# Optimization experiments

Hardware: AMD Instinct MI355X
Metric: run time of the kernel (lower is better)

Reference implementation:

```python
import jax, jax.numpy as jnp
import numpy as np

B, S, D = 2, 2048, 2048
H, G = 32, 8            # n_head, n_kv_groups
DH = D // H             # 64
HG = H // G             # heads per group = 4


def setup_inputs() -> dict:
    key = jax.random.key(0)
    ks = jax.random.split(key, 7)
    kv_dim = G * DH
    return {
        "q": jax.random.normal(ks[0], (B, S, D), jnp.float32),
        "k": jax.random.normal(ks[1], (B, S, D), jnp.float32),
        "v": jax.random.normal(ks[2], (B, S, D), jnp.float32),
        "mask": jnp.tril(jnp.ones((S, S), jnp.bool_)),  # causal
        "w_q": jax.random.normal(ks[3], (D, D), jnp.float32) * 0.02,
        "w_k": jax.random.normal(ks[4], (kv_dim, D), jnp.float32) * 0.02,
        "w_v": jax.random.normal(ks[5], (kv_dim, D), jnp.float32) * 0.02,
        "w_out": jax.random.normal(ks[6], (D, D), jnp.float32) * 0.02,
    }


def reference(q, k, v, mask, w_q, w_k, w_v, w_out):
    scale = 1.0 / np.sqrt(DH).astype(np.float32)
    # projections (F.linear: x @ W.T)
    qp = (q @ w_q.T).reshape(B, S, G, HG, DH)   # [b s g h d]
    kp = (k @ w_k.T).reshape(B, S, G, DH)       # [b t g d]
    vp = (v @ w_v.T).reshape(B, S, G, DH)
    # grouped attention scores [b g h s t]
    scores = jnp.einsum('bsghd,btgd->bghst', qp, kp) * scale
    scores = jnp.where(mask[None, None, None], scores, jnp.float32(-jnp.inf))
    attn = jax.nn.softmax(scores, axis=-1)
    out = jnp.einsum('bghst,btgd->bsghd', attn, vp).reshape(B, S, D)
    return out @ w_out.T
```

## Files before the change

### kernel.cpp

```cpp
#include <hip/hip_runtime.h>
#include <hip/hip_bf16.h>
#include <stdint.h>

#define B_SZ 2
#define S_LEN 2048
#define D_MODEL 2048
#define NH 32
#define NG 8
#define HGRP 4
#define DHEAD 64
#define KV_DIM 512
#define M_TOK 4096
#define KVB 64
#define QBLK 256
#define N_ITEMS2 768

typedef __attribute__((ext_vector_type(8))) short bf16x8;
typedef __attribute__((ext_vector_type(4))) float f32x4;
typedef __attribute__((ext_vector_type(16))) float f32x16;

__device__ inline unsigned short f2bf(float x) {
    uint32_t u = __builtin_bit_cast(uint32_t, x);
    uint32_t r = (u + 0x7fffu + ((u >> 16) & 1u)) >> 16;
    return (unsigned short)r;
}

__device__ inline uint32_t cvtpk(float lo, float hi) {
    uint32_t r;
    asm("v_cvt_pk_bf16_f32 %0, %1, %2" : "=v"(r) : "v"(lo), "v"(hi));
    return r;
}

__device__ inline void plswap(uint32_t& a, uint32_t& b) {
    asm volatile("v_permlane32_swap_b32 %0, %1" : "+v"(a), "+v"(b));
}

__device__ inline float bf2f(unsigned short u) {
    uint32_t x = ((uint32_t)u) << 16;
    return __builtin_bit_cast(float, x);
}

__device__ inline void async_copy16(const void* g, void* l) {
    __builtin_amdgcn_global_load_lds(
        (const __attribute__((address_space(1))) void*)g,
        (__attribute__((address_space(3))) void*)l,
        16, 0, 0);
}

__device__ inline void gbar() {
    asm volatile("" ::: "memory");
    __builtin_amdgcn_s_barrier();
    asm volatile("" ::: "memory");
}
__device__ inline void lgkm0() {
    asm volatile("s_waitcnt lgkmcnt(0)" ::: "memory");
    __builtin_amdgcn_sched_barrier(0);
}

__global__ __launch_bounds__(256) void cvt_all(const float* __restrict__ q,
                                               const float* __restrict__ k,
                                               const float* __restrict__ v,
                                               const float* __restrict__ wq,
                                               const float* __restrict__ wk,
                                               const float* __restrict__ wv,
                                               const float* __restrict__ wo,
                                               unsigned short* __restrict__ qb,
                                               unsigned short* __restrict__ kb,
                                               unsigned short* __restrict__ vb,
                                               unsigned short* __restrict__ wqb,
                                               unsigned short* __restrict__ wkvb,
                                               unsigned short* __restrict__ wob,
                                               unsigned int* __restrict__ cnt) {
    const int i = blockIdx.x * 256 + threadIdx.x;
    if (i == 0) *cnt = 0u;
    const float* src; unsigned short* dst; int j;
    if (i < 1048576)      { src = q;  dst = qb;  j = i; }
    else if (i < 2097152) { src = k;  dst = kb;  j = i - 1048576; }
    else if (i < 3145728) { src = v;  dst = vb;  j = i - 2097152; }
    else if (i < 3670016) { src = wq; dst = wqb; j = i - 3145728; }
    else if (i < 3801088) { src = wk; dst = wkvb; j = i - 3670016; }
    else if (i < 3932160) { src = wv; dst = wkvb + (size_t)KV_DIM * D_MODEL; j = i - 3801088; }
    else                  { src = wo; dst = wob; j = i - 3932160; }
    const float4* p = reinterpret_cast<const float4*>(src) + (size_t)j * 2;
    float4 a = p[0], b = p[1];
    union { unsigned short u[8]; uint4 v4; } r;
    r.u[0] = f2bf(a.x); r.u[1] = f2bf(a.y); r.u[2] = f2bf(a.z); r.u[3] = f2bf(a.w);
    r.u[4] = f2bf(b.x); r.u[5] = f2bf(b.y); r.u[6] = f2bf(b.z); r.u[7] = f2bf(b.w);
    reinterpret_cast<uint4*>(dst)[j] = r.v4;
}

#define SCALE_Q 0.1803368867f
#define GK 2048

__global__ __launch_bounds__(512, 2) void gemm8p(const unsigned short* __restrict__ Aq,
                                                 const unsigned short* __restrict__ Ak,
                                                 const unsigned short* __restrict__ Av,
                                                 const unsigned short* __restrict__ Bq,
                                                 const unsigned short* __restrict__ Bkv,
                                                 unsigned short* __restrict__ out_q,
                                                 unsigned short* __restrict__ out_k,
                                                 unsigned short* __restrict__ out_v) {
    __shared__ __align__(16) char lds[131072];

    const int tid = threadIdx.x;
    const int lane = tid & 63;
    const int w = tid >> 6;
    const int wm = w >> 2, wn = w & 3;
    const int l15 = lane & 15, l4 = lane >> 4;

    int bid = blockIdx.x;
    bid = (bid & 7) * 24 + (bid >> 3);
    const int mb = bid & 15, nb = bid >> 4;
    const int m0 = mb * 256;

    const unsigned short* Ap;
    const unsigned short* Bp;
    int mode = 0, n0q = 0;
    if (nb < 8) {
        Ap = Aq; Bp = Bq + (size_t)(nb * 256) * GK; mode = 0; n0q = nb * 256;
    } else if (nb < 10) {
        Ap = Ak; Bp = Bkv + (size_t)((nb - 8) * 256) * GK; mode = 1; n0q = (nb - 8) * 256;
    } else {
        Ap = Av; Bp = Bkv + (size_t)((nb - 10) * 256 + 512) * GK; mode = 2; n0q = (nb - 10) * 256;
    }

    const int srow = tid >> 3;
    const int gcol = (((tid & 7) * 16) ^ ((srow & 7) << 4)) >> 1;
    char* const myl = lds + tid * 16;

    auto stageA = [&](int tile, int half) {
        char* dst = myl + (tile & 1) * 32768 + half * 16384;
        const unsigned short* src = Ap + (size_t)(m0 + half * 128 + srow) * GK + tile * 64 + gcol;
        async_copy16(src, dst);
        async_copy16(src + (size_t)64 * GK, dst + 8192);
    };
    auto stageB = [&](int tile, int half) {
        char* dst = myl + 65536 + (tile & 1) * 32768 + half * 16384;
        const unsigned short* src = Bp + (size_t)(half * 128 + srow) * GK + tile * 64 + gcol;
        async_copy16(src, dst);
        async_copy16(src + (size_t)64 * GK, dst + 8192);
    };

    bf16x8 af[4][2], bf[4][2];
    auto loadA = [&](int buf, int mhalf) {
        const char* base = lds + buf * 32768;
#pragma unroll
        for (int mi = 0; mi < 4; ++mi) {
            const int r = wm * 128 + mhalf * 64 + mi * 16 + l15;
#pragma unroll
            for (int ks = 0; ks < 2; ++ks)
                af[mi][ks] = *reinterpret_cast<const bf16x8*>(
                    base + r * 128 + ((ks * 64 + l4 * 16) ^ ((r & 7) << 4)));
        }
    };
    auto loadB = [&](int buf, int nhalf) {
        const char* base = lds + 65536 + buf * 32768;
#pragma unroll
        for (int ni2 = 0; ni2 < 2; ++ni2) {
            const int ni = nhalf * 2 + ni2;
            const int r = wn * 64 + ni * 16 + l15;
#pragma unroll
            for (int ks = 0; ks < 2; ++ks)
                bf[ni][ks] = *reinterpret_cast<const bf16x8*>(
                    base + r * 128 + ((ks * 64 + l4 * 16) ^ ((r & 7) << 4)));
        }
    };

    f32x4 acc[8][4] = {};
    auto mfma16 = [&](int mq, int nq) {
        __builtin_amdgcn_s_setprio(1);
#pragma unroll
        for (int mi = 0; mi < 4; ++mi)
#pragma unroll
            for (int ni2 = 0; ni2 < 2; ++ni2)
#pragma unroll
                for (int ks = 0; ks < 2; ++ks)
                    acc[mq * 4 + mi][nq * 2 + ni2] = __builtin_amdgcn_mfma_f32_16x16x32_bf16(
                        af[mi][ks], bf[nq * 2 + ni2][ks], acc[mq * 4 + mi][nq * 2 + ni2], 0, 0, 0);
        __builtin_amdgcn_s_setprio(0);
    };

    stageA(0, 0); stageA(0, 1); stageB(0, 0); stageB(0, 1); stageB(1, 0); stageB(1, 1);
    asm volatile("s_waitcnt vmcnt(4)" ::: "memory");
    gbar();

    for (int i = 0; i < 16; ++i) {
        const int u = 2 * i;
        const bool nl = (i < 15);
        loadA(0, 0); loadB(0, 0); stageA(u + 1, 0);
        gbar(); lgkm0(); mfma16(0, 0); gbar();
        loadB(0, 1); stageA(u + 1, 1);
        gbar(); lgkm0(); mfma16(0, 1); gbar();
        loadA(0, 1); if (nl) stageB(u + 2, 0);
        gbar(); lgkm0(); mfma16(1, 0); gbar();
        if (nl) stageB(u + 2, 1);
        gbar(); mfma16(1, 1);
        if (nl) asm volatile("s_waitcnt vmcnt(4)" ::: "memory");
        else    asm volatile("s_waitcnt vmcnt(0)" ::: "memory");
        gbar();
        loadA(1, 0); loadB(1, 0); if (nl) stageA(u + 2, 0);
        gbar(); lgkm0(); mfma16(0, 0); gbar();
        loadB(1, 1); if (nl) stageA(u + 2, 1);
        gbar(); lgkm0(); mfma16(0, 1); gbar();
        loadA(1, 1); if (nl) stageB(u + 3, 0);
        gbar(); lgkm0(); mfma16(1, 0); gbar();
        if (nl) stageB(u + 3, 1);
        gbar(); mfma16(1, 1);
        if (nl) asm volatile("s_waitcnt vmcnt(4)" ::: "memory");
        gbar();
    }

    if (mode == 0) {
#pragma unroll
        for (int mi = 0; mi < 8; ++mi) {
            const int row = m0 + wm * 128 + mi * 16 + l4 * 4;
#pragma unroll
            for (int ni = 0; ni < 4; ++ni) {
                const int col = n0q + wn * 64 + ni * 16 + l15;
#pragma unroll
                for (int r = 0; r < 4; ++r)
                    out_q[(size_t)(row + r) * D_MODEL + col] = f2bf(acc[mi][ni][r] * SCALE_Q);
            }
        }
    } else if (mode == 1) {
#pragma unroll
        for (int mi = 0; mi < 8; ++mi) {
            const int row = m0 + wm * 128 + mi * 16 + l4 * 4;
#pragma unroll
            for (int ni = 0; ni < 4; ++ni) {
                const int col = n0q + wn * 64 + ni * 16 + l15;
#pragma unroll
                for (int r = 0; r < 4; ++r)
                    out_k[(size_t)(row + r) * KV_DIM + col] = f2bf(acc[mi][ni][r]);
            }
        }
    } else {
        const int bb = m0 >> 11;
#pragma unroll
        for (int mi = 0; mi < 8; ++mi) {
            const int tok = (m0 & 2047) + wm * 128 + mi * 16 + l4 * 4;
#pragma unroll
            for (int ni = 0; ni < 4; ++ni) {
                const int c = n0q + wn * 64 + ni * 16 + l15;
                const int g = c >> 6, dh = c & 63;
                uint2 pk;
                pk.x = cvtpk(acc[mi][ni][0], acc[mi][ni][1]);
                pk.y = cvtpk(acc[mi][ni][2], acc[mi][ni][3]);
                *reinterpret_cast<uint2*>(out_v + (size_t)((bb * NG + g) * DHEAD + dh) * S_LEN + tok) = pk;
            }
        }
    }
}

__global__ __launch_bounds__(512, 1) void gemm8o(const unsigned short* __restrict__ A,
                                                 const unsigned short* __restrict__ B,
                                                 float* __restrict__ C) {
    __shared__ __align__(16) char lds[98304];

    const int tid = threadIdx.x;
    const int lane = tid & 63;
    const int w = tid >> 6;
    const int wm = w >> 1, wn = w & 1;
    const int l15 = lane & 15, l4 = lane >> 4;

    int bid = blockIdx.x;
    bid = (bid & 7) * 32 + (bid >> 3);
    const int mb = bid & 15, nb = bid >> 4;
    const int m0 = mb * 256, n0 = nb * 128;
    const unsigned short* Bp = B + (size_t)n0 * GK;

    const int srow = tid >> 3;
    const int gcol = (((tid & 7) * 16) ^ ((srow & 7) << 4)) >> 1;

    auto stageA = [&](int tile, int half) {
        char* dst = lds + (tile & 1) * 32768 + half * 16384 + tid * 16;
        const unsigned short* src = A + (size_t)(m0 + half * 128 + srow) * GK + tile * 64 + gcol;
        async_copy16(src, dst);
        async_copy16(src + (size_t)64 * GK, dst + 8192);
    };
    auto stageB = [&](int tile, int half) {
        char* dst = lds + 65536 + (tile & 1) * 16384 + half * 8192 + tid * 16;
        const unsigned short* src = Bp + (size_t)(half * 64 + srow) * GK + tile * 64 + gcol;
        async_copy16(src, dst);
    };

    bf16x8 af[2][2], bf[4][2];
    auto loadA2 = [&](int buf, int mhalf) {
        const char* base = lds + buf * 32768;
#pragma unroll
        for (int mi = 0; mi < 2; ++mi) {
            const int r = wm * 64 + mhalf * 32 + mi * 16 + l15;
#pragma unroll
            for (int ks = 0; ks < 2; ++ks)
                af[mi][ks] = *reinterpret_cast<const bf16x8*>(
                    base + r * 128 + ((ks * 64 + l4 * 16) ^ ((r & 7) << 4)));
        }
    };
    auto loadB2 = [&](int buf, int nhalf) {
        const char* base = lds + 65536 + buf * 16384;
#pragma unroll
        for (int ni2 = 0; ni2 < 2; ++ni2) {
            const int ni = nhalf * 2 + ni2;
            const int r = wn * 64 + ni * 16 + l15;
#pragma unroll
            for (int ks = 0; ks < 2; ++ks)
                bf[ni][ks] = *reinterpret_cast<const bf16x8*>(
                    base + r * 128 + ((ks * 64 + l4 * 16) ^ ((r & 7) << 4)));
        }
    };

    f32x4 acc[4][4] = {};
    auto mfma8 = [&](int mq, int nq) {
        __builtin_amdgcn_s_setprio(1);
#pragma unroll
        for (int mi = 0; mi < 2; ++mi)
#pragma unroll
            for (int ni2 = 0; ni2 < 2; ++ni2)
#pragma unroll
                for (int ks = 0; ks < 2; ++ks)
                    acc[mq * 2 + mi][nq * 2 + ni2] = __builtin_amdgcn_mfma_f32_16x16x32_bf16(
                        af[mi][ks], bf[nq * 2 + ni2][ks], acc[mq * 2 + mi][nq * 2 + ni2], 0, 0, 0);
        __builtin_amdgcn_s_setprio(0);
    };

    stageA(0, 0); stageA(0, 1); stageB(0, 0); stageB(0, 1); stageB(1, 0); stageB(1, 1);
    asm volatile("s_waitcnt vmcnt(2)" ::: "memory");
    gbar();

    for (int i = 0; i < 16; ++i) {
        const int u = 2 * i;
        const bool nl = (i < 15);
        loadA2(0, 0); loadB2(0, 0); stageA(u + 1, 0);
        gbar(); lgkm0(); mfma8(0, 0); gbar();
        loadB2(0, 1); stageA(u + 1, 1);
        gbar(); lgkm0(); mfma8(0, 1); gbar();
        loadA2(0, 1); if (nl) stageB(u + 2, 0);
        gbar(); lgkm0(); mfma8(1, 0); gbar();
        if (nl) stageB(u + 2, 1);
        gbar(); mfma8(1, 1);
        if (nl) asm volatile("s_waitcnt vmcnt(2)" ::: "memory");
        else    asm volatile("s_waitcnt vmcnt(0)" ::: "memory");
        gbar();
        loadA2(1, 0); loadB2(1, 0); if (nl) stageA(u + 2, 0);
        gbar(); lgkm0(); mfma8(0, 0); gbar();
        loadB2(1, 1); if (nl) stageA(u + 2, 1);
        gbar(); lgkm0(); mfma8(0, 1); gbar();
        loadA2(1, 1); if (nl) stageB(u + 3, 0);
        gbar(); lgkm0(); mfma8(1, 0); gbar();
        if (nl) stageB(u + 3, 1);
        gbar(); mfma8(1, 1);
        if (nl) asm volatile("s_waitcnt vmcnt(2)" ::: "memory");
        gbar();
    }

#pragma unroll
    for (int mi = 0; mi < 4; ++mi) {
        const int row = m0 + wm * 64 + mi * 16 + l4 * 4;
#pragma unroll
        for (int ni = 0; ni < 4; ++ni) {
            const int col = n0 + wn * 64 + ni * 16 + l15;
#pragma unroll
            for (int r = 0; r < 4; ++r)
                C[(size_t)(row + r) * D_MODEL + col] = acc[mi][ni][r];
        }
    }
}

__constant__ unsigned char cls2_qi[12]   = {7,7,3,6,6,5,5,2,4,4,1,0};
__constant__ unsigned char cls2_half[12] = {0,1,0,0,1,0,1,0,0,1,0,0};

__global__ __launch_bounds__(512, 4) void attn3_kernel(const unsigned short* __restrict__ qp,
                                                       const unsigned short* __restrict__ kp,
                                                       const unsigned short* __restrict__ vpT,
                                                       unsigned short* __restrict__ attn_out,
                                                       unsigned int* __restrict__ counter,
                                                       unsigned short* __restrict__ partO,
                                                       float* __restrict__ ml) {
    __shared__ __align__(16) unsigned short Ks[2][KVB * 64];
    __shared__ __align__(16) unsigned short Vs[2][KVB * 64];
    __shared__ int s_item;

    const int tid = threadIdx.x;
    const int lane = tid & 63;
    const int w = tid >> 6;
    const int l31 = lane & 31, hi = lane >> 5;
    const int sr = tid >> 3, sc = tid & 7;
    const int sgcol = (((sc * 16) ^ ((sr & 7) << 4)) >> 1);
    char* const kdst0 = (char*)Ks[0] + tid * 16;
    char* const kdst1 = (char*)Ks[1] + tid * 16;
    char* const vdst0 = (char*)Vs[0] + tid * 16;
    char* const vdst1 = (char*)Vs[1] + tid * 16;

    for (;;) {
        if (tid == 0) s_item = (int)atomicAdd(counter, 1u);
        __syncthreads();
        const int item = s_item;
        if (item >= N_ITEMS2) break;
        const int slot = item >> 6;
        const int bh = item & 63;
        const int qi = cls2_qi[slot];
        const int half = cls2_half[slot];
        const bool split = qi >= 4;
        const int b = bh >> 5, head = bh & 31, g = head >> 2;
        const int s0 = qi * QBLK;
        const int m = s0 + w * 32 + l31;
        const int mmaxw = s0 + w * 32 + 31;

        int j0, j1;
        if (split) { j0 = half * 2 * (qi + 1); j1 = j0 + 2 * (qi + 1); }
        else       { j0 = 0;                   j1 = 4 * (qi + 1); }

        bf16x8 qf[4];
        {
            const unsigned short* qrow = qp + (size_t)(b * S_LEN + m) * D_MODEL + head * DHEAD + hi * 8;
#pragma unroll
            for (int k = 0; k < 4; ++k)
                qf[k] = *reinterpret_cast<const bf16x8*>(qrow + k * 16);
        }

        const unsigned short* kbase = kp + (size_t)(b * S_LEN + sr) * KV_DIM + g * DHEAD + sgcol;
        const unsigned short* vbase = vpT + (size_t)((b * NG + g) * DHEAD + sr) * S_LEN + sgcol;

        float mrun = -1e30f, lrun = 0.f;
        f32x16 o0 = {}, o1 = {};

        async_copy16(kbase + (size_t)j0 * KVB * KV_DIM, kdst0);
        async_copy16(vbase + j0 * KVB, vdst0);
        asm volatile("s_waitcnt vmcnt(0)" ::: "memory");
        gbar();

        for (int j = j0; j < j1; ++j) {
            const int cur = (j - j0) & 1;
            const int t0 = j * KVB;
            if (j + 1 < j1) {
                async_copy16(kbase + (size_t)(j + 1) * KVB * KV_DIM, cur ? kdst0 : kdst1);
                async_copy16(vbase + (j + 1) * KVB, cur ? vdst0 : vdst1);
            }

            const bool tt0 = (t0 <= mmaxw);
            const bool tt1 = (t0 + 32 <= mmaxw);
            if (tt0) {
                const char* Kb = (const char*)Ks[cur];
                const char* Vb = (const char*)Vs[cur];
                const int rswz0 = (l31 & 7) << 4;

                f32x16 s0v = {}, s1v = {};
#pragma unroll
                for (int k = 0; k < 4; ++k) {
                    const int coff = k * 32 + hi * 16;
                    const bf16x8 kf0 = *reinterpret_cast<const bf16x8*>(
                        Kb + l31 * 128 + (coff ^ rswz0));
                    s0v = __builtin_amdgcn_mfma_f32_32x32x16_bf16(kf0, qf[k], s0v, 0, 0, 0);
                    if (tt1) {
                        const bf16x8 kf1 = *reinterpret_cast<const bf16x8*>(
                            Kb + (32 + l31) * 128 + (coff ^ rswz0));
                        s1v = __builtin_amdgcn_mfma_f32_32x32x16_bf16(kf1, qf[k], s1v, 0, 0, 0);
                    }
                }

                const bool msk = (t0 + KVB - 1) > (s0 + w * 32);
                float rmax = -1e30f;
                if (msk) {
#pragma unroll
                    for (int r = 0; r < 16; ++r) {
                        const int tloc = (r & 3) + 8 * (r >> 2) + 4 * hi;
                        float v = s0v[r];
                        if (t0 + tloc > m) v = -1e30f;
                        s0v[r] = v;
                        rmax = fmaxf(rmax, v);
                    }
                    if (tt1) {
#pragma unroll
                        for (int r = 0; r < 16; ++r) {
                            const int tloc = 32 + (r & 3) + 8 * (r >> 2) + 4 * hi;
                            float v = s1v[r];
                            if (t0 + tloc > m) v = -1e30f;
                            s1v[r] = v;
                            rmax = fmaxf(rmax, v);
                        }
                    }
                } else {
#pragma unroll
                    for (int r = 0; r < 16; ++r)
                        rmax = fmaxf(rmax, s0v[r]);
                    if (tt1) {
#pragma unroll
                        for (int r = 0; r < 16; ++r)
                            rmax = fmaxf(rmax, s1v[r]);
                    }
                }
                rmax = fmaxf(rmax, __shfl_xor(rmax, 32, 64));
                if (!__all(rmax <= mrun + 8.0f)) {
                    const float mnew = fmaxf(mrun, rmax);
                    const float corr = __builtin_amdgcn_exp2f(mrun - mnew);
                    lrun *= corr;
#pragma unroll
                    for (int r = 0; r < 16; ++r) { o0[r] *= corr; o1[r] *= corr; }
                    mrun = mnew;
                }
                float rs = 0.f;
#pragma unroll
                for (int r = 0; r < 16; ++r) {
                    const float p = __builtin_amdgcn_exp2f(s0v[r] - mrun);
                    s0v[r] = p;
                    rs += p;
                }
                if (tt1) {
#pragma unroll
                    for (int r = 0; r < 16; ++r) {
                        const float p = __builtin_amdgcn_exp2f(s1v[r] - mrun);
                        s1v[r] = p;
                        rs += p;
                    }
                }
                rs += __shfl_xor(rs, 32, 64);
                lrun += rs;

#pragma unroll
                for (int c = 0; c < 4; ++c) {
                    if (c >= 2 && !tt1) break;
                    const f32x16& sv = (c >> 1) ? s1v : s0v;
                    const int h8 = (c & 1) * 8;
                    uint32_t a0 = cvtpk(sv[h8 + 0], sv[h8 + 1]);
                    uint32_t a1 = cvtpk(sv[h8 + 2], sv[h8 + 3]);
                    uint32_t b0 = cvtpk(sv[h8 + 4], sv[h8 + 5]);
                    uint32_t b1 = cvtpk(sv[h8 + 6], sv[h8 + 7]);
                    plswap(a0, b0); plswap(a1, b1);
                    union { uint32_t w4[4]; bf16x8 v; } pf;
                    pf.w4[0] = a0; pf.w4[1] = a1; pf.w4[2] = b0; pf.w4[3] = b1;
                    const int coff = c * 32 + hi * 16;
                    const bf16x8 vf0 = *reinterpret_cast<const bf16x8*>(
                        Vb + l31 * 128 + (coff ^ rswz0));
                    o0 = __builtin_amdgcn_mfma_f32_32x32x16_bf16(vf0, pf.v, o0, 0, 0, 0);
                    const bf16x8 vf1 = *reinterpret_cast<const bf16x8*>(
                        Vb + (32 + l31) * 128 + (coff ^ rswz0));
                    o1 = __builtin_amdgcn_mfma_f32_32x32x16_bf16(vf1, pf.v, o1, 0, 0, 0);
                }
            }
            asm volatile("s_waitcnt vmcnt(0)" ::: "memory");
            gbar();
        }

        if (split) {
            const int pb = ((bh << 2) + (qi - 4)) * 2 + half;
            const int mrow = w * 32 + l31;
            if (hi == 0) {
                ml[pb * 512 + mrow] = mrun;
                ml[pb * 512 + 256 + mrow] = lrun;
            }
            unsigned short* dst = partO + (size_t)pb * 16384 + mrow * 64 + hi * 4;
#pragma unroll
            for (int qd = 0; qd < 4; ++qd) {
                uint2 pk0, pk1;
                pk0.x = cvtpk(o0[4 * qd + 0], o0[4 * qd + 1]);
                pk0.y = cvtpk(o0[4 * qd + 2], o0[4 * qd + 3]);
                pk1.x = cvtpk(o1[4 * qd + 0], o1[4 * qd + 1]);
                pk1.y = cvtpk(o1[4 * qd + 2], o1[4 * qd + 3]);
                *reinterpret_cast<uint2*>(dst + 8 * qd) = pk0;
                *reinterpret_cast<uint2*>(dst + 32 + 8 * qd) = pk1;
            }
        } else {
            const float inv = 1.0f / lrun;
            unsigned short* dst = attn_out + (size_t)(b * S_LEN + m) * D_MODEL + head * DHEAD + hi * 4;
#pragma unroll
            for (int qd = 0; qd < 4; ++qd) {
                uint2 pk0, pk1;
                pk0.x = cvtpk(o0[4 * qd + 0] * inv, o0[4 * qd + 1] * inv);
                pk0.y = cvtpk(o0[4 * qd + 2] * inv, o0[4 * qd + 3] * inv);
                pk1.x = cvtpk(o1[4 * qd + 0] * inv, o1[4 * qd + 1] * inv);
                pk1.y = cvtpk(o1[4 * qd + 2] * inv, o1[4 * qd + 3] * inv);
                *reinterpret_cast<uint2*>(dst + 8 * qd) = pk0;
                *reinterpret_cast<uint2*>(dst + 32 + 8 * qd) = pk1;
            }
        }
    }
}

__global__ __launch_bounds__(512) void merge2_kernel(const unsigned short* __restrict__ partO,
                                                     const float* __restrict__ ml,
                                                     unsigned short* __restrict__ attn_out) {
    const int blk = blockIdx.x;
    const int bh = blk >> 2;
    const int qi = (blk & 3) + 4;
    const int b = bh >> 5, head = bh & 31;
    const int s0 = qi * QBLK;
    const int tid = threadIdx.x;
    const int row = tid >> 1, dh0 = (tid & 1) * 32;
    const int pb0 = blk * 2, pb1 = pb0 + 1;

    const float m0 = ml[pb0 * 512 + row], l0 = ml[pb0 * 512 + 256 + row];
    const float m1 = ml[pb1 * 512 + row], l1 = ml[pb1 * 512 + 256 + row];
    const float M = fmaxf(m0, m1);
    float w0 = __builtin_amdgcn_exp2f(m0 - M);
    float w1 = __builtin_amdgcn_exp2f(m1 - M);
    const float inv = 1.0f / (l0 * w0 + l1 * w1);
    w0 *= inv; w1 *= inv;

    const uint4* p0 = reinterpret_cast<const uint4*>(partO + (size_t)pb0 * 16384 + row * 64 + dh0);
    const uint4* p1 = reinterpret_cast<const uint4*>(partO + (size_t)pb1 * 16384 + row * 64 + dh0);
    unsigned short* dst = attn_out + (size_t)(b * S_LEN + s0 + row) * D_MODEL + head * DHEAD + dh0;
#pragma unroll
    for (int c = 0; c < 4; ++c) {
        union { unsigned short u[8]; uint4 v; } ua, ub, uo;
        ua.v = p0[c]; ub.v = p1[c];
#pragma unroll
        for (int e = 0; e < 8; e += 2) {
            float x0 = bf2f(ua.u[e]) * w0 + bf2f(ub.u[e]) * w1;
            float x1 = bf2f(ua.u[e + 1]) * w0 + bf2f(ub.u[e + 1]) * w1;
            reinterpret_cast<uint32_t*>(uo.u)[e >> 1] = cvtpk(x0, x1);
        }
        reinterpret_cast<uint4*>(dst)[c] = uo.v;
    }
}

extern "C" void kernel_launch(void* const* d_in, const int* in_sizes, int n_in,
                              void* d_out, int out_size, void* d_ws, size_t ws_size,
                              hipStream_t stream) {
    const float* q     = (const float*)d_in[0];
    const float* k     = (const float*)d_in[1];
    const float* v     = (const float*)d_in[2];
    const float* w_q   = (const float*)d_in[4];
    const float* w_k   = (const float*)d_in[5];
    const float* w_v   = (const float*)d_in[6];
    const float* w_out = (const float*)d_in[7];

    char* ws = (char*)d_ws;
    size_t off = 0;
    auto alloc = [&](size_t n) { char* p = ws + off; off += (n + 255) & ~(size_t)255; return p; };
    unsigned short* qb   = (unsigned short*)alloc((size_t)M_TOK * D_MODEL * 2);
    unsigned short* kb   = (unsigned short*)alloc((size_t)M_TOK * D_MODEL * 2);
    unsigned short* vb   = (unsigned short*)alloc((size_t)M_TOK * D_MODEL * 2);
    unsigned short* wqb  = (unsigned short*)alloc((size_t)D_MODEL * D_MODEL * 2);
    unsigned short* wkvb = (unsigned short*)alloc((size_t)2 * KV_DIM * D_MODEL * 2);
    unsigned short* wob  = (unsigned short*)alloc((size_t)D_MODEL * D_MODEL * 2);
    unsigned short* qpb  = (unsigned short*)alloc((size_t)M_TOK * D_MODEL * 2);
    unsigned short* kpb  = (unsigned short*)alloc((size_t)M_TOK * KV_DIM * 2);
    unsigned short* vtb  = (unsigned short*)alloc((size_t)M_TOK * KV_DIM * 2);
    unsigned short* aob  = (unsigned short*)alloc((size_t)M_TOK * D_MODEL * 2);
    float*          mlb  = (float*)alloc((size_t)512 * 512 * 4);
    unsigned int*   cnt  = (unsigned int*)alloc(256);

    cvt_all<<<dim3(17408), dim3(256), 0, stream>>>(q, k, v, w_q, w_k, w_v, w_out,
                                                   qb, kb, vb, wqb, wkvb, wob, cnt);

    gemm8p<<<dim3(192), dim3(512), 0, stream>>>(qb, kb, vb, wqb, wkvb, qpb, kpb, vtb);

    attn3_kernel<<<dim3(768), dim3(512), 0, stream>>>(qpb, kpb, vtb, aob, cnt, qb, mlb);
    merge2_kernel<<<dim3(256), dim3(512), 0, stream>>>(qb, mlb, aob);

    gemm8o<<<dim3(256), dim3(512), 0, stream>>>(aob, wob, (float*)d_out);
}
```

Baseline: 189.3 us.

## Split causal attention into finer equal-size KV chunks with multi-part merge

Replaces the two-way split of the longest query blocks with a schedule of 1280 work items. Each item covers at most about 8 KV tiles, and every query block from index 2 upward is split into 2 to 4 partial results. A new merge kernel combines up to 4 partials using their running max and sum. The aim is to balance load across workgroups and shrink the tail, at the cost of more partial-output traffic and merge work. It also restructures the row max and sum reductions as trees, and reuses the kb/qb workspace buffers for the partials and the max/sum values.

```diff
diff --git a/kernel.cpp b/kernel.cpp
--- a/kernel.cpp
+++ b/kernel.cpp
@@ -13,7 +13,7 @@
 #define M_TOK 4096
 #define KVB 64
 #define QBLK 256
-#define N_ITEMS2 768
+#define N_ITEMS 1280
 
 typedef __attribute__((ext_vector_type(8))) short bf16x8;
 typedef __attribute__((ext_vector_type(4))) float f32x4;
@@ -55,6 +55,22 @@
 __device__ inline void lgkm0() {
     asm volatile("s_waitcnt lgkmcnt(0)" ::: "memory");
     __builtin_amdgcn_sched_barrier(0);
+}
+
+__device__ inline float vmax16(const f32x16& v) {
+    float a0 = fmaxf(v[0], v[1]), a1 = fmaxf(v[2], v[3]);
+    float a2 = fmaxf(v[4], v[5]), a3 = fmaxf(v[6], v[7]);
+    float a4 = fmaxf(v[8], v[9]), a5 = fmaxf(v[10], v[11]);
+    float a6 = fmaxf(v[12], v[13]), a7 = fmaxf(v[14], v[15]);
+    float b0 = fmaxf(a0, a1), b1 = fmaxf(a2, a3);
+    float b2 = fmaxf(a4, a5), b3 = fmaxf(a6, a7);
+    return fmaxf(fmaxf(b0, b1), fmaxf(b2, b3));
+}
+__device__ inline float vsum16(const f32x16& v) {
+    float a0 = v[0] + v[1], a1 = v[2] + v[3], a2 = v[4] + v[5], a3 = v[6] + v[7];
+    float a4 = v[8] + v[9], a5 = v[10] + v[11], a6 = v[12] + v[13], a7 = v[14] + v[15];
+    float b0 = a0 + a1, b1 = a2 + a3, b2 = a4 + a5, b3 = a6 + a7;
+    return (b0 + b1) + (b2 + b3);
 }
 
 __global__ __launch_bounds__(256) void cvt_all(const float* __restrict__ q,
@@ -366,10 +382,14 @@
     }
 }
 
-__constant__ unsigned char cls2_qi[12]   = {7,7,3,6,6,5,5,2,4,4,1,0};
-__constant__ unsigned char cls2_half[12] = {0,1,0,0,1,0,1,0,0,1,0,0};
-
-__global__ __launch_bounds__(512, 4) void attn3_kernel(const unsigned short* __restrict__ qp,
+__constant__ unsigned char sl_qi[20] = {7,7,7,7, 5,5,5, 3,3, 1, 6,6,6,6, 4,4,4, 2,2, 0};
+__constant__ unsigned char sl_j0[20] = {0,8,16,24, 0,8,16, 0,8, 0, 0,7,14,21, 0,7,14, 0,6, 0};
+__constant__ unsigned char sl_j1[20] = {8,16,24,32, 8,16,24, 8,16, 8, 7,14,21,28, 7,14,20, 6,12, 4};
+__constant__ unsigned char sl_pt[20] = {0,1,2,3, 0,1,2, 0,1, 0, 0,1,2,3, 0,1,2, 0,1, 0};
+__constant__ unsigned char pb_base[6] = {16,14,11,8,4,0};
+__constant__ unsigned char np_tab[6]  = {2,2,3,3,4,4};
+
+__global__ __launch_bounds__(512, 4) void attn7_kernel(const unsigned short* __restrict__ qp,
                                                        const unsigned short* __restrict__ kp,
                                                        const unsigned short* __restrict__ vpT,
                                                        unsigned short* __restrict__ attn_out,
@@ -395,20 +415,19 @@
         if (tid == 0) s_item = (int)atomicAdd(counter, 1u);
         __syncthreads();
         const int item = s_item;
-        if (item >= N_ITEMS2) break;
-        const int slot = item >> 6;
+        if (item >= N_ITEMS) break;
+        const int slot = item / 64;
         const int bh = item & 63;
-        const int qi = cls2_qi[slot];
-        const int half = cls2_half[slot];
-        const bool split = qi >= 4;
+        const int qi = sl_qi[slot];
+        const int j0 = sl_j0[slot];
+        const int j1 = sl_j1[slot];
+        const int part = sl_pt[slot];
+        const bool merged = (qi >= 2);
         const int b = bh >> 5, head = bh & 31, g = head >> 2;
         const int s0 = qi * QBLK;
         const int m = s0 + w * 32 + l31;
-        const int mmaxw = s0 + w * 32 + 31;
-
-        int j0, j1;
-        if (split) { j0 = half * 2 * (qi + 1); j1 = j0 + 2 * (qi + 1); }
-        else       { j0 = 0;                   j1 = 4 * (qi + 1); }
+        const int mmin = s0 + w * 32;
+        const int mmaxw = mmin + 31;
 
         bf16x8 qf[4];
         {
@@ -458,37 +477,23 @@
                     }
                 }
 
-                const bool msk = (t0 + KVB - 1) > (s0 + w * 32);
-                float rmax = -1e30f;
+                const bool msk = (t0 + KVB - 1) > mmin;
                 if (msk) {
 #pragma unroll
                     for (int r = 0; r < 16; ++r) {
                         const int tloc = (r & 3) + 8 * (r >> 2) + 4 * hi;
-                        float v = s0v[r];
-                        if (t0 + tloc > m) v = -1e30f;
-                        s0v[r] = v;
-                        rmax = fmaxf(rmax, v);
+                        if (t0 + tloc > m) s0v[r] = -1e30f;
                     }
                     if (tt1) {
 #pragma unroll
                         for (int r = 0; r < 16; ++r) {
                             const int tloc = 32 + (r & 3) + 8 * (r >> 2) + 4 * hi;
-                            float v = s1v[r];
-                            if (t0 + tloc > m) v = -1e30f;
-                            s1v[r] = v;
-                            rmax = fmaxf(rmax, v);
+                            if (t0 + tloc > m) s1v[r] = -1e30f;
                         }
                     }
-                } else {
-#pragma unroll
-                    for (int r = 0; r < 16; ++r)
-                        rmax = fmaxf(rmax, s0v[r]);
-                    if (tt1) {
-#pragma unroll
-                        for (int r = 0; r < 16; ++r)
-                            rmax = fmaxf(rmax, s1v[r]);
-                    }
                 }
+                float rmax = vmax16(s0v);
+                if (tt1) rmax = fmaxf(rmax, vmax16(s1v));
                 rmax = fmaxf(rmax, __shfl_xor(rmax, 32, 64));
                 if (!__all(rmax <= mrun + 8.0f)) {
                     const float mnew = fmaxf(mrun, rmax);
@@ -498,21 +503,16 @@
                     for (int r = 0; r < 16; ++r) { o0[r] *= corr; o1[r] *= corr; }
                     mrun = mnew;
                 }
-                float rs = 0.f;
-#pragma unroll
-                for (int r = 0; r < 16; ++r) {
-                    const float p = __builtin_amdgcn_exp2f(s0v[r] - mrun);
-                    s0v[r] = p;
-                    rs += p;
+#pragma unroll
+                for (int r = 0; r < 16; ++r)
+                    s0v[r] = __builtin_amdgcn_exp2f(s0v[r] - mrun);
+                if (tt1) {
+#pragma unroll
+                    for (int r = 0; r < 16; ++r)
+                        s1v[r] = __builtin_amdgcn_exp2f(s1v[r] - mrun);
                 }
-                if (tt1) {
-#pragma unroll
-                    for (int r = 0; r < 16; ++r) {
-                        const float p = __builtin_amdgcn_exp2f(s1v[r] - mrun);
-                        s1v[r] = p;
-                        rs += p;
-                    }
-                }
+                float rs = vsum16(s0v);
+                if (tt1) rs += vsum16(s1v);
                 rs += __shfl_xor(rs, 32, 64);
                 lrun += rs;
 
@@ -541,8 +541,8 @@
             gbar();
         }
 
-        if (split) {
-            const int pb = ((bh << 2) + (qi - 4)) * 2 + half;
+        if (merged) {
+            const int pb = bh * 18 + pb_base[qi - 2] + part;
             const int mrow = w * 32 + l31;
             if (hi == 0) {
                 ml[pb * 512 + mrow] = mrun;
@@ -576,39 +576,56 @@
     }
 }
 
-__global__ __launch_bounds__(512) void merge2_kernel(const unsigned short* __restrict__ partO,
+__global__ __launch_bounds__(512) void merge5_kernel(const unsigned short* __restrict__ partO,
                                                      const float* __restrict__ ml,
                                                      unsigned short* __restrict__ attn_out) {
     const int blk = blockIdx.x;
-    const int bh = blk >> 2;
-    const int qi = (blk & 3) + 4;
+    const int bh = blk / 6;
+    const int qi = 2 + (blk - bh * 6);
+    const int np = np_tab[qi - 2];
+    const int pb = bh * 18 + pb_base[qi - 2];
     const int b = bh >> 5, head = bh & 31;
     const int s0 = qi * QBLK;
     const int tid = threadIdx.x;
     const int row = tid >> 1, dh0 = (tid & 1) * 32;
-    const int pb0 = blk * 2, pb1 = pb0 + 1;
-
-    const float m0 = ml[pb0 * 512 + row], l0 = ml[pb0 * 512 + 256 + row];
-    const float m1 = ml[pb1 * 512 + row], l1 = ml[pb1 * 512 + 256 + row];
-    const float M = fmaxf(m0, m1);
-    float w0 = __builtin_amdgcn_exp2f(m0 - M);
-    float w1 = __builtin_amdgcn_exp2f(m1 - M);
-    const float inv = 1.0f / (l0 * w0 + l1 * w1);
-    w0 *= inv; w1 *= inv;
-
-    const uint4* p0 = reinterpret_cast<const uint4*>(partO + (size_t)pb0 * 16384 + row * 64 + dh0);
-    const uint4* p1 = reinterpret_cast<const uint4*>(partO + (size_t)pb1 * 16384 + row * 64 + dh0);
+
+    float mv[4], lv[4];
+#pragma unroll
+    for (int i = 0; i < 4; ++i) {
+        if (i < np) { mv[i] = ml[(pb + i) * 512 + row]; lv[i] = ml[(pb + i) * 512 + 256 + row]; }
+        else        { mv[i] = -1e30f; lv[i] = 0.f; }
+    }
+    const float M = fmaxf(fmaxf(mv[0], mv[1]), fmaxf(mv[2], mv[3]));
+    float wgt[4];
+    float denom = 0.f;
+#pragma unroll
+    for (int i = 0; i < 4; ++i) {
+        wgt[i] = (i < np) ? __builtin_amdgcn_exp2f(mv[i] - M) : 0.f;
+        denom += lv[i] * wgt[i];
+    }
+    const float inv = 1.0f / denom;
+#pragma unroll
+    for (int i = 0; i < 4; ++i) wgt[i] *= inv;
+
     unsigned short* dst = attn_out + (size_t)(b * S_LEN + s0 + row) * D_MODEL + head * DHEAD + dh0;
 #pragma unroll
     for (int c = 0; c < 4; ++c) {
-        union { unsigned short u[8]; uint4 v; } ua, ub, uo;
-        ua.v = p0[c]; ub.v = p1[c];
-#pragma unroll
-        for (int e = 0; e < 8; e += 2) {
-            float x0 = bf2f(ua.u[e]) * w0 + bf2f(ub.u[e]) * w1;
-            float x1 = bf2f(ua.u[e + 1]) * w0 + bf2f(ub.u[e + 1]) * w1;
-            reinterpret_cast<uint32_t*>(uo.u)[e >> 1] = cvtpk(x0, x1);
-        }
+        float x[8] = {};
+#pragma unroll
+        for (int i = 0; i < 4; ++i) {
+            if (i < np) {
+                union { unsigned short u[8]; uint4 v; } ua;
+                ua.v = reinterpret_cast<const uint4*>(
+                    partO + (size_t)(pb + i) * 16384 + row * 64 + dh0)[c];
+#pragma unroll
+                for (int e = 0; e < 8; ++e)
+                    x[e] += bf2f(ua.u[e]) * wgt[i];
+            }
+        }
+        union { unsigned short u[8]; uint4 v; } uo;
+#pragma unroll
+        for (int e = 0; e < 8; e += 2)
+            reinterpret_cast<uint32_t*>(uo.u)[e >> 1] = cvtpk(x[e], x[e + 1]);
         reinterpret_cast<uint4*>(dst)[c] = uo.v;
     }
 }
@@ -637,7 +654,6 @@
     unsigned short* kpb  = (unsigned short*)alloc((size_t)M_TOK * KV_DIM * 2);
     unsigned short* vtb  = (unsigned short*)alloc((size_t)M_TOK * KV_DIM * 2);
     unsigned short* aob  = (unsigned short*)alloc((size_t)M_TOK * D_MODEL * 2);
-    float*          mlb  = (float*)alloc((size_t)512 * 512 * 4);
     unsigned int*   cnt  = (unsigned int*)alloc(256);
 
     cvt_all<<<dim3(17408), dim3(256), 0, stream>>>(q, k, v, w_q, w_k, w_v, w_out,
@@ -645,8 +661,8 @@
 
     gemm8p<<<dim3(192), dim3(512), 0, stream>>>(qb, kb, vb, wqb, wkvb, qpb, kpb, vtb);
 
-    attn3_kernel<<<dim3(768), dim3(512), 0, stream>>>(qpb, kpb, vtb, aob, cnt, qb, mlb);
-    merge2_kernel<<<dim3(256), dim3(512), 0, stream>>>(qb, mlb, aob);
+    attn7_kernel<<<dim3(1024), dim3(512), 0, stream>>>(qpb, kpb, vtb, aob, cnt, kb, (float*)qb);
+    merge5_kernel<<<dim3(384), dim3(512), 0, stream>>>(kb, (float*)qb, aob);
 
     gemm8o<<<dim3(256), dim3(512), 0, stream>>>(aob, wob, (float*)d_out);
 }
```

After: 217.6 us. 1.15x slower.
